# Kernel tuning notes

Measured on AMD Instinct MI355X. Metric: run time of the kernel, lower is better.

Reference implementation:

```python
import jax, jax.numpy as jnp
import numpy as np

B, IN, HID, EMB, K = 65536, 256, 256, 64, 4096
EPS = 1e-5  # BatchNorm1d default eps


def setup_inputs() -> dict:
    key = jax.random.key(0)
    ks = jax.random.split(key, 12)
    s = 0.05
    return {
        "x": jax.random.normal(ks[0], (B, IN), jnp.float32),
        "W1": jax.random.normal(ks[1], (HID, IN), jnp.float32) * s,
        "b1": jax.random.normal(ks[2], (HID,), jnp.float32) * s,
        "gamma": jnp.ones((HID,), jnp.float32),
        "beta": jnp.zeros((HID,), jnp.float32),
        "mean": jax.random.normal(ks[3], (HID,), jnp.float32) * s,
        "var": jax.random.uniform(ks[4], (HID,), jnp.float32, 0.5, 1.5),
        "W2": jax.random.normal(ks[5], (HID // 2, HID), jnp.float32) * s,
        "b2": jax.random.normal(ks[6], (HID // 2,), jnp.float32) * s,
        "W3": jax.random.normal(ks[7], (EMB, HID // 2), jnp.float32) * s,
        "b3": jax.random.normal(ks[8], (EMB,), jnp.float32) * s,
        "codebook": jax.random.normal(ks[9], (K, EMB), jnp.float32),
    }


def reference(x, W1, b1, gamma, beta, mean, var, W2, b2, W3, b3, codebook):
    # encoder: Linear -> BatchNorm1d (eval stats) -> ReLU -> Linear -> ReLU -> Linear -> Tanh
    h = x @ W1.T + b1                                   # [B, HID]
    h = (h - mean) * jax.lax.rsqrt(var + EPS) * gamma + beta
    h = jax.nn.relu(h)
    h = jax.nn.relu(h @ W2.T + b2)                      # [B, HID//2]
    z = jnp.tanh(h @ W3.T + b3)                         # [B, EMB]
    # squared-distance matrix: ||z||^2 + ||e||^2 - 2 z e^T  -> [B, K]
    d = (jnp.sum(z * z, axis=1, keepdims=True)
         + jnp.sum(codebook * codebook, axis=1)
         - 2.0 * (z @ codebook.T))
    return jnp.argmin(d, axis=1)                        # [B] int token indices
```

## Files before the change

### kernel.cpp

```cpp
#include <hip/hip_runtime.h>

#define IN_DIM  256
#define HID_DIM 256
#define H2_DIM  128
#define EMB_DIM 64
#define K_CODES 4096
#define EPS_BN  1e-5f


typedef _Float16 f16;
typedef _Float16 f16x4 __attribute__((ext_vector_type(4)));
typedef _Float16 f16x8 __attribute__((ext_vector_type(8)));
typedef float    f32x16 __attribute__((ext_vector_type(16)));

__global__ __launch_bounds__(256) void k_norms(const float* __restrict__ cb,
                                               float* __restrict__ norms) {
    int c = blockIdx.x * 256 + threadIdx.x;
    const float4* row = reinterpret_cast<const float4*>(cb + (size_t)c * EMB_DIM);
    float s = 0.f;
#pragma unroll
    for (int i = 0; i < EMB_DIM / 4; ++i) {
        float4 v = row[i];
        s += v.x * v.x + v.y * v.y + v.z * v.z + v.w * v.w;
    }
    norms[c] = 0.5f * s;
}

__global__ __launch_bounds__(256) void k_prep(
    const float* __restrict__ W1, const float* __restrict__ W2,
    const float* __restrict__ W3, const float* __restrict__ cb,
    f16* __restrict__ p1h, f16* __restrict__ p1l,
    f16* __restrict__ p2h, f16* __restrict__ p2l,
    f16* __restrict__ p3h, f16* __restrict__ p3l,
    f16* __restrict__ cfh, f16* __restrict__ cfl) {
    int t = blockIdx.x * 256 + threadIdx.x;
    const float* src; f16 *dh, *dl; int tt, row, k0, K;
    if (t < 8192) {
        tt = t; int f = tt >> 6, l = tt & 63;
        int ct = f & 7, kst = f >> 3;
        row = ct * 32 + (l & 31); k0 = kst * 16 + (l >> 5) * 8;
        src = W1; K = IN_DIM; dh = p1h; dl = p1l;
    } else if (t < 12288) {
        tt = t - 8192; int f = tt >> 6, l = tt & 63;
        int ct = f & 3, kst = f >> 2;
        row = ct * 32 + (l & 31); k0 = kst * 16 + (l >> 5) * 8;
        src = W2; K = HID_DIM; dh = p2h; dl = p2l;
    } else if (t < 13312) {
        tt = t - 12288; int f = tt >> 6, l = tt & 63;
        int ct = f & 1, ks = f >> 1;
        row = ct * 32 + (l & 31); k0 = ks * 16 + (l >> 5) * 8;
        src = W3; K = H2_DIM; dh = p3h; dl = p3l;
    } else {
        tt = t - 13312; int f = tt >> 6, l = tt & 63;
        int ct = f & 3, ks = (f >> 2) & 3, ch = f >> 4;
        row = ch * 128 + ct * 32 + (l & 31); k0 = ks * 16 + (l >> 5) * 8;
        src = cb; K = EMB_DIM; dh = cfh; dl = cfl;
    }
    const float* s = src + (size_t)row * K + k0;
    f16x8 hv, lv;
#pragma unroll
    for (int j = 0; j < 8; ++j) {
        float v = s[j];
        f16 h = (f16)v;
        hv[j] = h;
        lv[j] = (f16)(v - (float)h);
    }
    *(f16x8*)(dh + (size_t)tt * 8) = hv;
    *(f16x8*)(dl + (size_t)tt * 8) = lv;
}

__global__ __launch_bounds__(256) void k_encoder_mfma(
    const float* __restrict__ x,
    const f16* __restrict__ p1h, const f16* __restrict__ p1l,
    const f16* __restrict__ p2h, const f16* __restrict__ p2l,
    const f16* __restrict__ p3h, const f16* __restrict__ p3l,
    const float* __restrict__ b1,
    const float* __restrict__ gm, const float* __restrict__ bt,
    const float* __restrict__ mu, const float* __restrict__ vr,
    const float* __restrict__ b2, const float* __restrict__ b3,
    f16* __restrict__ Zh, f16* __restrict__ Zl) {
    __shared__ __align__(16) f16 sm[25600];
    const int tid  = threadIdx.x;
    const int lane = tid & 63;
    const int w    = tid >> 6;
    const int ln31 = lane & 31;
    const int q    = lane >> 5;
    const int r0   = blockIdx.x * 32;

#pragma unroll
    for (int it = 0; it < 8; ++it) {
        int i = it * 256 + tid;
        int row = i >> 6, c4 = (i & 63) * 4;
        float4 v = *reinterpret_cast<const float4*>(
            x + (size_t)(r0 + row) * IN_DIM + c4);
        f16x4 hv, lv;
        hv[0] = (f16)v.x; lv[0] = (f16)(v.x - (float)hv[0]);
        hv[1] = (f16)v.y; lv[1] = (f16)(v.y - (float)hv[1]);
        hv[2] = (f16)v.z; lv[2] = (f16)(v.z - (float)hv[2]);
        hv[3] = (f16)v.w; lv[3] = (f16)(v.w - (float)hv[3]);
        *(f16x4*)(sm + row * 264 + c4)        = hv;
        *(f16x4*)(sm + 8448 + row * 264 + c4) = lv;
    }
    __syncthreads();

    f32x16 acc1a = {};
    f32x16 acc1b = {};
    {
        const f16* q1h = p1h + (size_t)(2 * w) * 512 + lane * 8;
        const f16* q1l = p1l + (size_t)(2 * w) * 512 + lane * 8;
        f16x8 bh0 = *(const f16x8*)(q1h);
        f16x8 bh1 = *(const f16x8*)(q1h + 512);
        f16x8 bl0 = *(const f16x8*)(q1l);
        f16x8 bl1 = *(const f16x8*)(q1l + 512);
#pragma unroll 2
        for (int kst = 0; kst < 16; ++kst) {
            f16x8 ch0 = bh0, ch1 = bh1, cl0 = bl0, cl1 = bl1;
            int kn = (kst + 1) & 15;
            bh0 = *(const f16x8*)(q1h + (size_t)kn * 4096);
            bh1 = *(const f16x8*)(q1h + (size_t)kn * 4096 + 512);
            bl0 = *(const f16x8*)(q1l + (size_t)kn * 4096);
            bl1 = *(const f16x8*)(q1l + (size_t)kn * 4096 + 512);
            int koff = kst * 16 + q * 8;
            f16x8 ah = *(const f16x8*)(sm + ln31 * 264 + koff);
            f16x8 al = *(const f16x8*)(sm + 8448 + ln31 * 264 + koff);
            acc1a = __builtin_amdgcn_mfma_f32_32x32x16_f16(ah, ch0, acc1a, 0, 0, 0);
            acc1b = __builtin_amdgcn_mfma_f32_32x32x16_f16(ah, ch1, acc1b, 0, 0, 0);
            acc1a = __builtin_amdgcn_mfma_f32_32x32x16_f16(al, ch0, acc1a, 0, 0, 0);
            acc1b = __builtin_amdgcn_mfma_f32_32x32x16_f16(al, ch1, acc1b, 0, 0, 0);
            acc1a = __builtin_amdgcn_mfma_f32_32x32x16_f16(ah, cl0, acc1a, 0, 0, 0);
            acc1b = __builtin_amdgcn_mfma_f32_32x32x16_f16(ah, cl1, acc1b, 0, 0, 0);
        }
    }
    __syncthreads();

    {
#pragma unroll
        for (int nt = 0; nt < 2; ++nt) {
            int j = w * 64 + nt * 32 + ln31;
            float sc = gm[j] * rsqrtf(vr[j] + EPS_BN);
            float sh = (b1[j] - mu[j]) * sc + bt[j];
            const f32x16& a = nt ? acc1b : acc1a;
#pragma unroll
            for (int r = 0; r < 16; ++r) {
                int row = (r & 3) + 8 * (r >> 2) + 4 * q;
                float v = a[r] * sc + sh;
                v = v > 0.f ? v : 0.f;
                f16 h = (f16)v;
                sm[row * 264 + j]        = h;
                sm[8448 + row * 264 + j] = (f16)(v - (float)h);
            }
        }
    }
    __syncthreads();

    f32x16 acc2a = {};
    f32x16 acc2b = {};
    {
        const f16* q2h = p2h + (size_t)w * 512 + lane * 8;
        const f16* q2l = p2l + (size_t)w * 512 + lane * 8;
        f16x8 bh = *(const f16x8*)(q2h);
        f16x8 bl = *(const f16x8*)(q2l);
#pragma unroll 2
        for (int kst = 0; kst < 16; ++kst) {
            f16x8 cbh = bh, cbl = bl;
            int kn = (kst + 1) & 15;
            bh = *(const f16x8*)(q2h + (size_t)kn * 2048);
            bl = *(const f16x8*)(q2l + (size_t)kn * 2048);
            int koff = kst * 16 + q * 8;
            f16x8 ah = *(const f16x8*)(sm + ln31 * 264 + koff);
            f16x8 al = *(const f16x8*)(sm + 8448 + ln31 * 264 + koff);
            f32x16& acc = (kst & 1) ? acc2b : acc2a;
            acc = __builtin_amdgcn_mfma_f32_32x32x16_f16(ah, cbh, acc, 0, 0, 0);
            acc = __builtin_amdgcn_mfma_f32_32x32x16_f16(al, cbh, acc, 0, 0, 0);
            acc = __builtin_amdgcn_mfma_f32_32x32x16_f16(ah, cbl, acc, 0, 0, 0);
        }
    }
    {
        int j2 = w * 32 + ln31;
        float bias = b2[j2];
#pragma unroll
        for (int r = 0; r < 16; ++r) {
            int row = (r & 3) + 8 * (r >> 2) + 4 * q;
            float v = (acc2a[r] + acc2b[r]) + bias;
            v = v > 0.f ? v : 0.f;
            f16 h = (f16)v;
            sm[16896 + row * 136 + j2] = h;
            sm[21248 + row * 136 + j2] = (f16)(v - (float)h);
        }
    }
    __syncthreads();

    if (w < 2) {
        f32x16 acc3a = {};
        f32x16 acc3b = {};
        const f16* q3h = p3h + (size_t)w * 512 + lane * 8;
        const f16* q3l = p3l + (size_t)w * 512 + lane * 8;
        f16x8 bh = *(const f16x8*)(q3h);
        f16x8 bl = *(const f16x8*)(q3l);
#pragma unroll 2
        for (int ks = 0; ks < 8; ++ks) {
            f16x8 cbh = bh, cbl = bl;
            int kn = (ks + 1) & 7;
            bh = *(const f16x8*)(q3h + (size_t)kn * 1024);
            bl = *(const f16x8*)(q3l + (size_t)kn * 1024);
            f16x8 ah = *(const f16x8*)(sm + 16896 + ln31 * 136 + ks * 16 + q * 8);
            f16x8 al = *(const f16x8*)(sm + 21248 + ln31 * 136 + ks * 16 + q * 8);
            f32x16& acc = (ks & 1) ? acc3b : acc3a;
            acc = __builtin_amdgcn_mfma_f32_32x32x16_f16(ah, cbh, acc, 0, 0, 0);
            acc = __builtin_amdgcn_mfma_f32_32x32x16_f16(al, cbh, acc, 0, 0, 0);
            acc = __builtin_amdgcn_mfma_f32_32x32x16_f16(ah, cbl, acc, 0, 0, 0);
        }
        int j3 = w * 32 + ln31;
        float bias = b3[j3];
#pragma unroll
        for (int r = 0; r < 16; ++r) {
            int row = (r & 3) + 8 * (r >> 2) + 4 * q;
            float zv = tanhf((acc3a[r] + acc3b[r]) + bias);
            f16 h = (f16)zv;
            size_t idx = (size_t)(r0 + row) * EMB_DIM + j3;
            Zh[idx] = h;
            Zl[idx] = (f16)(zv - (float)h);
        }
    }
}

__global__ __launch_bounds__(512) void k_argmin_mfma(
    const f16* __restrict__ Zh, const f16* __restrict__ Zl,
    const f16* __restrict__ cfh, const f16* __restrict__ cfl,
    const float* __restrict__ norms, int* __restrict__ out) {
    __shared__ __align__(16) f16 sm[16896];
    f16* ebh = sm;
    f16* ebl = sm + 8192;
    float* nbuf = (float*)(sm + 16384);
    const int tid  = threadIdx.x;
    const int lane = tid & 63;
    const int w    = tid >> 6;
    const int rt   = w & 3;
    const int hp   = w >> 2;
    const int ln31 = lane & 31;
    const int q    = lane >> 5;
    const int r0   = blockIdx.x * 128;

    f16x8 ah[4], al[4];
#pragma unroll
    for (int ks = 0; ks < 4; ++ks) {
        size_t zoff = (size_t)(r0 + rt * 32 + ln31) * EMB_DIM + ks * 16 + q * 8;
        ah[ks] = *(const f16x8*)(Zh + zoff);
        al[ks] = *(const f16x8*)(Zl + zoff);
    }

    float bv[16];
    int   bi[16];
#pragma unroll
    for (int i = 0; i < 16; ++i) { bv[i] = -3.4e38f; bi[i] = 0; }

    for (int ch = 0; ch < K_CODES / 128; ++ch) {
        __syncthreads();
        const float4* sh = (const float4*)(cfh + (size_t)ch * 8192);
        const float4* sl = (const float4*)(cfl + (size_t)ch * 8192);
        float4* dh = (float4*)ebh;
        float4* dl = (float4*)ebl;
#pragma unroll
        for (int it = 0; it < 2; ++it) {
            dh[it * 512 + tid] = sh[it * 512 + tid];
            dl[it * 512 + tid] = sl[it * 512 + tid];
        }
        if (tid < 128) nbuf[tid] = norms[ch * 128 + tid];
        __syncthreads();

#pragma unroll 1
        for (int c2 = 0; c2 < 2; ++c2) {
            int ct = hp * 2 + c2;
            f16x8 bh[4], bl[4];
#pragma unroll
            for (int ks = 0; ks < 4; ++ks) {
                int off = (ks * 4 + ct) * 512 + lane * 8;
                bh[ks] = *(const f16x8*)(ebh + off);
                bl[ks] = *(const f16x8*)(ebl + off);
            }
            f32x16 acc0 = {};
            f32x16 acc1 = {};
#pragma unroll
            for (int ks = 0; ks < 4; ks += 2) {
                acc0 = __builtin_amdgcn_mfma_f32_32x32x16_f16(ah[ks],     bh[ks],     acc0, 0, 0, 0);
                acc1 = __builtin_amdgcn_mfma_f32_32x32x16_f16(ah[ks + 1], bh[ks + 1], acc1, 0, 0, 0);
                acc0 = __builtin_amdgcn_mfma_f32_32x32x16_f16(al[ks],     bh[ks],     acc0, 0, 0, 0);
                acc1 = __builtin_amdgcn_mfma_f32_32x32x16_f16(al[ks + 1], bh[ks + 1], acc1, 0, 0, 0);
                acc0 = __builtin_amdgcn_mfma_f32_32x32x16_f16(ah[ks],     bl[ks],     acc0, 0, 0, 0);
                acc1 = __builtin_amdgcn_mfma_f32_32x32x16_f16(ah[ks + 1], bl[ks + 1], acc1, 0, 0, 0);
            }
            float nv  = nbuf[ct * 32 + ln31];
            int   col = ch * 128 + ct * 32 + ln31;
#pragma unroll
            for (int r = 0; r < 16; ++r) {
                float t  = (acc0[r] + acc1[r]) - nv;
                bool  gt = t > bv[r];
                bv[r] = gt ? t : bv[r];
                bi[r] = gt ? col : bi[r];
            }
        }
    }

    __syncthreads();
    {
        float* pv = (float*)sm;
        int*   pi = (int*)sm + 4096;
        if (w >= 4) {
#pragma unroll
            for (int r = 0; r < 16; ++r) {
                pv[(w - 4) * 1024 + lane * 16 + r] = bv[r];
                pi[(w - 4) * 1024 + lane * 16 + r] = bi[r];
            }
        }
        __syncthreads();
        if (w < 4) {
#pragma unroll
            for (int r = 0; r < 16; ++r) {
                float v2 = pv[w * 1024 + lane * 16 + r];
                int   i2 = pi[w * 1024 + lane * 16 + r];
                bool tk = (v2 > bv[r]) || (v2 == bv[r] && i2 < bi[r]);
                bv[r] = tk ? v2 : bv[r];
                bi[r] = tk ? i2 : bi[r];
            }
        }
    }
    __syncthreads();

    float* redv = (float*)sm;
    int*   redi = (int*)sm + 4224;
    if (w < 4) {
#pragma unroll
        for (int r = 0; r < 16; ++r) {
            int row = (r & 3) + 8 * (r >> 2) + 4 * q + 32 * w;
            redv[row * 33 + ln31] = bv[r];
            redi[row * 33 + ln31] = bi[r];
        }
    }
    __syncthreads();
    if (tid < 128) {
        float v  = redv[tid * 33];
        int   ix = redi[tid * 33];
#pragma unroll
        for (int j = 1; j < 32; ++j) {
            float vj = redv[tid * 33 + j];
            int   ij = redi[tid * 33 + j];
            if (vj > v || (vj == v && ij < ix)) { v = vj; ix = ij; }
        }
        out[r0 + tid] = ix;
    }
}

extern "C" void kernel_launch(void* const* d_in, const int* in_sizes, int n_in,
                              void* d_out, int out_size, void* d_ws, size_t ws_size,
                              hipStream_t stream) {
    (void)n_in; (void)out_size; (void)ws_size;
    const float* x  = (const float*)d_in[0];
    const float* W1 = (const float*)d_in[1];
    const float* b1 = (const float*)d_in[2];
    const float* gm = (const float*)d_in[3];
    const float* bt = (const float*)d_in[4];
    const float* mu = (const float*)d_in[5];
    const float* vr = (const float*)d_in[6];
    const float* W2 = (const float*)d_in[7];
    const float* b2 = (const float*)d_in[8];
    const float* W3 = (const float*)d_in[9];
    const float* b3 = (const float*)d_in[10];
    const float* cb = (const float*)d_in[11];

    char* ws = (char*)d_ws;
    float* norms = (float*)ws;
    f16* cfh = (f16*)(ws + 16384);
    f16* cfl = (f16*)(ws + 540672);
    f16* p1h = (f16*)(ws + 1064960);
    f16* p1l = (f16*)(ws + 1196032);
    f16* p2h = (f16*)(ws + 1327104);
    f16* p2l = (f16*)(ws + 1392640);
    f16* p3h = (f16*)(ws + 1458176);
    f16* p3l = (f16*)(ws + 1474560);
    f16* Zh  = (f16*)(ws + 1490944);
    f16* Zl  = (f16*)(ws + 9879552);
    int* out = (int*)d_out;

    const int B = in_sizes[0] / IN_DIM;

    k_norms<<<K_CODES / 256, 256, 0, stream>>>(cb, norms);
    k_prep<<<180, 256, 0, stream>>>(W1, W2, W3, cb, p1h, p1l, p2h, p2l,
                                    p3h, p3l, cfh, cfl);
    k_encoder_mfma<<<B / 32, 256, 0, stream>>>(x, p1h, p1l, p2h, p2l, p3h, p3l,
                                               b1, gm, bt, mu, vr, b2, b3, Zh, Zl);
    k_argmin_mfma<<<B / 128, 512, 0, stream>>>(Zh, Zl, cfh, cfl, norms, out);
}
```

Baseline: 281.1 us.

## Give each argmin wave two row tiles to reuse codebook fragments

The argmin kernel drops from 512 to 256 threads per block, and each wave now handles two 32-row tiles of Z instead of one. Every codebook fragment read from shared memory feeds twice as many MFMAs, which halves LDS reads per FLOP. The exchange is roughly double the register use for Z fragments and running best values, which lowers occupancy and latency hiding. The merge buffers are reworked with padded strides to fit the new layout.

```diff
diff --git a/kernel.cpp b/kernel.cpp
--- a/kernel.cpp
+++ b/kernel.cpp
@@ -224,7 +224,7 @@
     }
 }
 
-__global__ __launch_bounds__(512) void k_argmin_mfma(
+__global__ __launch_bounds__(256) void k_argmin_mfma(
     const f16* __restrict__ Zh, const f16* __restrict__ Zl,
     const f16* __restrict__ cfh, const f16* __restrict__ cfl,
     const float* __restrict__ norms, int* __restrict__ out) {
@@ -235,25 +235,32 @@
     const int tid  = threadIdx.x;
     const int lane = tid & 63;
     const int w    = tid >> 6;
-    const int rt   = w & 3;
-    const int hp   = w >> 2;
+    const int rg   = w & 1;
+    const int hp   = w >> 1;
     const int ln31 = lane & 31;
     const int q    = lane >> 5;
     const int r0   = blockIdx.x * 128;
 
-    f16x8 ah[4], al[4];
+    f16x8 ah0[4], al0[4], ah1[4], al1[4];
 #pragma unroll
     for (int ks = 0; ks < 4; ++ks) {
-        size_t zoff = (size_t)(r0 + rt * 32 + ln31) * EMB_DIM + ks * 16 + q * 8;
-        ah[ks] = *(const f16x8*)(Zh + zoff);
-        al[ks] = *(const f16x8*)(Zl + zoff);
-    }
-
-    float bv[16];
-    int   bi[16];
-#pragma unroll
-    for (int i = 0; i < 16; ++i) { bv[i] = -3.4e38f; bi[i] = 0; }
-
+        size_t za = (size_t)(r0 + rg * 64 + ln31) * EMB_DIM + ks * 16 + q * 8;
+        size_t zb = za + (size_t)32 * EMB_DIM;
+        ah0[ks] = *(const f16x8*)(Zh + za);
+        al0[ks] = *(const f16x8*)(Zl + za);
+        ah1[ks] = *(const f16x8*)(Zh + zb);
+        al1[ks] = *(const f16x8*)(Zl + zb);
+    }
+
+    float bv0[16], bv1[16];
+    int   bi0[16], bi1[16];
+#pragma unroll
+    for (int i = 0; i < 16; ++i) {
+        bv0[i] = -3.4e38f; bi0[i] = 0;
+        bv1[i] = -3.4e38f; bi1[i] = 0;
+    }
+
+#pragma unroll 1
     for (int ch = 0; ch < K_CODES / 128; ++ch) {
         __syncthreads();
         const float4* sh = (const float4*)(cfh + (size_t)ch * 8192);
@@ -261,9 +268,9 @@
         float4* dh = (float4*)ebh;
         float4* dl = (float4*)ebl;
 #pragma unroll
-        for (int it = 0; it < 2; ++it) {
-            dh[it * 512 + tid] = sh[it * 512 + tid];
-            dl[it * 512 + tid] = sl[it * 512 + tid];
+        for (int it = 0; it < 4; ++it) {
+            dh[it * 256 + tid] = sh[it * 256 + tid];
+            dl[it * 256 + tid] = sl[it * 256 + tid];
         }
         if (tid < 128) nbuf[tid] = norms[ch * 128 + tid];
         __syncthreads();
@@ -278,25 +285,47 @@
                 bh[ks] = *(const f16x8*)(ebh + off);
                 bl[ks] = *(const f16x8*)(ebl + off);
             }
-            f32x16 acc0 = {};
-            f32x16 acc1 = {};
-#pragma unroll
-            for (int ks = 0; ks < 4; ks += 2) {
-                acc0 = __builtin_amdgcn_mfma_f32_32x32x16_f16(ah[ks],     bh[ks],     acc0, 0, 0, 0);
-                acc1 = __builtin_amdgcn_mfma_f32_32x32x16_f16(ah[ks + 1], bh[ks + 1], acc1, 0, 0, 0);
-                acc0 = __builtin_amdgcn_mfma_f32_32x32x16_f16(al[ks],     bh[ks],     acc0, 0, 0, 0);
-                acc1 = __builtin_amdgcn_mfma_f32_32x32x16_f16(al[ks + 1], bh[ks + 1], acc1, 0, 0, 0);
-                acc0 = __builtin_amdgcn_mfma_f32_32x32x16_f16(ah[ks],     bl[ks],     acc0, 0, 0, 0);
-                acc1 = __builtin_amdgcn_mfma_f32_32x32x16_f16(ah[ks + 1], bl[ks + 1], acc1, 0, 0, 0);
-            }
             float nv  = nbuf[ct * 32 + ln31];
             int   col = ch * 128 + ct * 32 + ln31;
-#pragma unroll
-            for (int r = 0; r < 16; ++r) {
-                float t  = (acc0[r] + acc1[r]) - nv;
-                bool  gt = t > bv[r];
-                bv[r] = gt ? t : bv[r];
-                bi[r] = gt ? col : bi[r];
+            {
+                f32x16 acc0 = {};
+                f32x16 acc1 = {};
+#pragma unroll
+                for (int ks = 0; ks < 4; ks += 2) {
+                    acc0 = __builtin_amdgcn_mfma_f32_32x32x16_f16(ah0[ks],     bh[ks],     acc0, 0, 0, 0);
+                    acc1 = __builtin_amdgcn_mfma_f32_32x32x16_f16(ah0[ks + 1], bh[ks + 1], acc1, 0, 0, 0);
+                    acc0 = __builtin_amdgcn_mfma_f32_32x32x16_f16(al0[ks],     bh[ks],     acc0, 0, 0, 0);
+                    acc1 = __builtin_amdgcn_mfma_f32_32x32x16_f16(al0[ks + 1], bh[ks + 1], acc1, 0, 0, 0);
+                    acc0 = __builtin_amdgcn_mfma_f32_32x32x16_f16(ah0[ks],     bl[ks],     acc0, 0, 0, 0);
+                    acc1 = __builtin_amdgcn_mfma_f32_32x32x16_f16(ah0[ks + 1], bl[ks + 1], acc1, 0, 0, 0);
+                }
+#pragma unroll
+                for (int r = 0; r < 16; ++r) {
+                    float t  = (acc0[r] + acc1[r]) - nv;
+                    bool  gt = t > bv0[r];
+                    bv0[r] = gt ? t : bv0[r];
+                    bi0[r] = gt ? col : bi0[r];
+                }
+            }
+            {
+                f32x16 acc0 = {};
+                f32x16 acc1 = {};
+#pragma unroll
+                for (int ks = 0; ks < 4; ks += 2) {
+                    acc0 = __builtin_amdgcn_mfma_f32_32x32x16_f16(ah1[ks],     bh[ks],     acc0, 0, 0, 0);
+                    acc1 = __builtin_amdgcn_mfma_f32_32x32x16_f16(ah1[ks + 1], bh[ks + 1], acc1, 0, 0, 0);
+                    acc0 = __builtin_amdgcn_mfma_f32_32x32x16_f16(al1[ks],     bh[ks],     acc0, 0, 0, 0);
+                    acc1 = __builtin_amdgcn_mfma_f32_32x32x16_f16(al1[ks + 1], bh[ks + 1], acc1, 0, 0, 0);
+                    acc0 = __builtin_amdgcn_mfma_f32_32x32x16_f16(ah1[ks],     bl[ks],     acc0, 0, 0, 0);
+                    acc1 = __builtin_amdgcn_mfma_f32_32x32x16_f16(ah1[ks + 1], bl[ks + 1], acc1, 0, 0, 0);
+                }
+#pragma unroll
+                for (int r = 0; r < 16; ++r) {
+                    float t  = (acc0[r] + acc1[r]) - nv;
+                    bool  gt = t > bv1[r];
+                    bv1[r] = gt ? t : bv1[r];
+                    bi1[r] = gt ? col : bi1[r];
+                }
             }
         }
     }
@@ -304,23 +333,30 @@
     __syncthreads();
     {
         float* pv = (float*)sm;
-        int*   pi = (int*)sm + 4096;
-        if (w >= 4) {
+        int*   pi = (int*)sm + 4224;
+        if (hp == 1) {
 #pragma unroll
             for (int r = 0; r < 16; ++r) {
-                pv[(w - 4) * 1024 + lane * 16 + r] = bv[r];
-                pi[(w - 4) * 1024 + lane * 16 + r] = bi[r];
+                pv[rg * 2112 + lane * 33 + r]      = bv0[r];
+                pi[rg * 2112 + lane * 33 + r]      = bi0[r];
+                pv[rg * 2112 + lane * 33 + 16 + r] = bv1[r];
+                pi[rg * 2112 + lane * 33 + 16 + r] = bi1[r];
             }
         }
         __syncthreads();
-        if (w < 4) {
+        if (hp == 0) {
 #pragma unroll
             for (int r = 0; r < 16; ++r) {
-                float v2 = pv[w * 1024 + lane * 16 + r];
-                int   i2 = pi[w * 1024 + lane * 16 + r];
-                bool tk = (v2 > bv[r]) || (v2 == bv[r] && i2 < bi[r]);
-                bv[r] = tk ? v2 : bv[r];
-                bi[r] = tk ? i2 : bi[r];
+                float v2 = pv[rg * 2112 + lane * 33 + r];
+                int   i2 = pi[rg * 2112 + lane * 33 + r];
+                bool tk = (v2 > bv0[r]) || (v2 == bv0[r] && i2 < bi0[r]);
+                bv0[r] = tk ? v2 : bv0[r];
+                bi0[r] = tk ? i2 : bi0[r];
+                float v3 = pv[rg * 2112 + lane * 33 + 16 + r];
+                int   i3 = pi[rg * 2112 + lane * 33 + 16 + r];
+                bool tk1 = (v3 > bv1[r]) || (v3 == bv1[r] && i3 < bi1[r]);
+                bv1[r] = tk1 ? v3 : bv1[r];
+                bi1[r] = tk1 ? i3 : bi1[r];
             }
         }
     }
@@ -328,12 +364,16 @@
 
     float* redv = (float*)sm;
     int*   redi = (int*)sm + 4224;
-    if (w < 4) {
+    if (hp == 0) {
 #pragma unroll
         for (int r = 0; r < 16; ++r) {
-            int row = (r & 3) + 8 * (r >> 2) + 4 * q + 32 * w;
-            redv[row * 33 + ln31] = bv[r];
-            redi[row * 33 + ln31] = bi[r];
+            int rowm = (r & 3) + 8 * (r >> 2) + 4 * q;
+            int row0 = rg * 64 + rowm;
+            int row1 = rg * 64 + 32 + rowm;
+            redv[row0 * 33 + ln31] = bv0[r];
+            redi[row0 * 33 + ln31] = bi0[r];
+            redv[row1 * 33 + ln31] = bv1[r];
+            redi[row1 * 33 + ln31] = bi1[r];
         }
     }
     __syncthreads();
@@ -388,5 +428,5 @@
                                     p3h, p3l, cfh, cfl);
     k_encoder_mfma<<<B / 32, 256, 0, stream>>>(x, p1h, p1l, p2h, p2l, p3h, p3l,
                                                b1, gm, bt, mu, vr, b2, b3, Zh, Zl);
-    k_argmin_mfma<<<B / 128, 512, 0, stream>>>(Zh, Zl, cfh, cfl, norms, out);
+    k_argmin_mfma<<<B / 128, 256, 0, stream>>>(Zh, Zl, cfh, cfl, norms, out);
 }
```

After: 385.4 us. 1.37x slower.
